# Performance work log

Hardware: AMD Instinct MI355X
Metric: run time of the kernel (lower is better)

Reference implementation:

```python
import jax, jax.numpy as jnp
import numpy as np

B, N, D = 8, 1024, 1024

def setup_inputs() -> dict:
    key = jax.random.key(0)
    k1, k2, k3, k4, k5 = jax.random.split(key, 5)
    x = jax.random.normal(k1, (B, N, D), dtype=jnp.float32)
    y = jax.random.normal(k2, (B, N, D), dtype=jnp.float32)
    adj = jax.random.uniform(k3, (B, N, N), dtype=jnp.float32)
    adj_sumrow = jnp.sum(adj, axis=-1, keepdims=True)  # [B, N, 1], row-sum normalizer
    W = jax.random.normal(k4, (D, D), dtype=jnp.float32) * (1.0 / np.sqrt(D))
    b = jax.random.normal(k5, (D,), dtype=jnp.float32) * 0.02
    return {"x": x, "y": y, "adj": adj, "adj_sumrow": adj_sumrow, "W": W, "b": b}

def reference(x, y, adj, adj_sumrow, W, b):
    # GraphConvolutionCustom: project neighbor features, aggregate via dense adj,
    # normalize by row-sum, add bias and residual input x; then ReLU.
    # Dropout is identity in eval mode (training=False).
    support = jnp.einsum('bnd,de->bne', y, W)          # [B, N, D]
    agg = jnp.matmul(adj, support) / adj_sumrow        # [B, N, D]
    out = jax.nn.relu(agg + b + x)
    return out
```

## Files before the change

### kernel.cpp

```cpp
#include <hip/hip_runtime.h>
#include <hip/hip_bf16.h>
#include <stdint.h>


typedef float  f32x4  __attribute__((ext_vector_type(4)));
typedef __bf16 bf16x8 __attribute__((ext_vector_type(8)));

__device__ __forceinline__ unsigned short f2bf(float f) {
  union { float f; unsigned int u; } c; c.f = f;
  unsigned int u = c.u;
  u += 0x7FFFu + ((u >> 16) & 1u);
  return (unsigned short)(u >> 16);
}

__device__ __forceinline__ void async_cp16(const void* g, void* l) {
  __builtin_amdgcn_global_load_lds(
      (const __attribute__((address_space(1))) unsigned int*)g,
      (__attribute__((address_space(3))) unsigned int*)l, 16, 0, 0);
}

__device__ __forceinline__ void bar() { asm volatile("s_barrier" ::: "memory"); }
#define VMCNT(n) asm volatile("s_waitcnt vmcnt(" #n ")" ::: "memory")


__global__ __launch_bounds__(256) void k_prep(
    const float4* __restrict__ y4, const float4* __restrict__ a4,
    ushort4* __restrict__ yb, ushort4* __restrict__ ab,
    const float* __restrict__ W, unsigned short* __restrict__ Wt)
{
  __shared__ float t[64][65];
  const int bid = blockIdx.x;
  if (bid < 16384) {
    const int i = bid * 256 + threadIdx.x;
    const bool isY = i < 2097152;
    const float4 v = isY ? y4[i] : a4[i - 2097152];
    ushort4 p;
    p.x = f2bf(v.x); p.y = f2bf(v.y); p.z = f2bf(v.z); p.w = f2bf(v.w);
    if (isY) yb[i] = p; else ab[i - 2097152] = p;
  } else {
    const int id = bid - 16384;
    const int n0 = (id & 15) * 64, k0 = (id >> 4) * 64;
    const int tx = threadIdx.x & 63, ty = threadIdx.x >> 6;
#pragma unroll
    for (int r = ty; r < 64; r += 4)
      t[r][tx] = W[(size_t)(k0 + r) * 1024 + n0 + tx];
    __syncthreads();
#pragma unroll
    for (int r = ty; r < 64; r += 4)
      Wt[(size_t)(n0 + r) * 1024 + k0 + tx] = f2bf(t[tx][r]);
  }
}


__device__ __forceinline__ void stageA(
    const unsigned short* __restrict__ A, int sA, int m0, int k0, int c,
    unsigned short* la, int wave, int rg, int colo)
{
#pragma unroll
  for (int s = 0; s < 2; ++s) {
    const int t = wave * 2 + s;
    const int row0 = (t >> 3) * 128 + c * 64 + (t & 7) * 8;
    async_cp16(A + (size_t)(m0 + row0 + rg) * sA + k0 + colo, la + row0 * 64);
  }
}

__device__ __forceinline__ void stageB(
    const unsigned short* __restrict__ Bt, int sB, int n0, int k0, int c,
    unsigned short* lb, int wave, int rg, int colo)
{
#pragma unroll
  for (int s = 0; s < 2; ++s) {
    const int t = wave * 2 + s;
    const int row0 = (t >> 2) * 64 + c * 32 + (t & 3) * 8;
    async_cp16(Bt + (size_t)(n0 + row0 + rg) * sB + k0 + colo, lb + row0 * 64);
  }
}

__device__ __forceinline__ void readA(
    const unsigned short* la, bf16x8 af[2][4], int wm, int mh, int quad, int l16)
{
#pragma unroll
  for (int h = 0; h < 2; ++h)
#pragma unroll
    for (int i = 0; i < 4; ++i) {
      const int r = wm + mh * 64 + i * 16 + l16;
      af[h][i] = *(const bf16x8*)(la + r * 64 + ((h * 4 + quad + r) & 7) * 8);
    }
}

__device__ __forceinline__ void readB(
    const unsigned short* lb, bf16x8 bfr[2][2], int wn, int nh, int quad, int l16)
{
#pragma unroll
  for (int h = 0; h < 2; ++h)
#pragma unroll
    for (int j = 0; j < 2; ++j) {
      const int r = wn + nh * 32 + j * 16 + l16;
      bfr[h][j] = *(const bf16x8*)(lb + r * 64 + ((h * 4 + quad + r) & 7) * 8);
    }
}

__device__ __forceinline__ void quad16(
    bf16x8 af[2][4], bf16x8 bfr[2][2], f32x4 acc[8][4], int mh, int nh)
{
  __builtin_amdgcn_s_setprio(1);
#pragma unroll
  for (int h = 0; h < 2; ++h)
#pragma unroll
    for (int i = 0; i < 4; ++i)
#pragma unroll
      for (int j = 0; j < 2; ++j)
        acc[mh * 4 + i][nh * 2 + j] = __builtin_amdgcn_mfma_f32_16x16x32_bf16(
            af[h][i], bfr[h][j], acc[mh * 4 + i][nh * 2 + j], 0, 0, 0);
  __builtin_amdgcn_s_setprio(0);
}

__device__ __forceinline__ void gemm256(
    const unsigned short* __restrict__ A,  int sA,
    const unsigned short* __restrict__ Bt, int sB,
    int m0, int n0, f32x4 acc[8][4], unsigned short* lsm, int tid)
{
  const int lane = tid & 63, wave = tid >> 6;
  const int wm = (wave >> 2) * 128, wn = (wave & 3) * 64;
  const int quad = lane >> 4, l16 = lane & 15;
  const int rg = lane >> 3;
  const int colo = (((lane & 7) - rg) & 7) * 8;

  bf16x8 af[2][4], bfr[2][2];

  stageA(A, sA, m0, 0, 0, lsm,        wave, rg, colo);
  stageB(Bt, sB, n0, 0, 0, lsm + 16384, wave, rg, colo);
  stageB(Bt, sB, n0, 0, 1, lsm + 16384, wave, rg, colo);
  stageA(A, sA, m0, 0, 1, lsm,        wave, rg, colo);

#pragma unroll 1
  for (int T = 0; T < 15; ++T) {
    const unsigned short* la = lsm + (T & 1) * 32768;
    const unsigned short* lb = la + 16384;
    unsigned short* na = lsm + ((T + 1) & 1) * 32768;
    unsigned short* nb = na + 16384;
    const int nk = (T + 1) * 64;

    VMCNT(4); bar();
    stageA(A, sA, m0, nk, 0, na, wave, rg, colo);
    readA(la, af, wm, 0, quad, l16);
    readB(lb, bfr, wn, 0, quad, l16);
    quad16(af, bfr, acc, 0, 0);

    VMCNT(4); bar();
    stageB(Bt, sB, n0, nk, 0, nb, wave, rg, colo);
    readB(lb, bfr, wn, 1, quad, l16);
    quad16(af, bfr, acc, 0, 1);

    VMCNT(4); bar();
    stageB(Bt, sB, n0, nk, 1, nb, wave, rg, colo);
    readA(la, af, wm, 1, quad, l16);
    quad16(af, bfr, acc, 1, 1);

    stageA(A, sA, m0, nk, 1, na, wave, rg, colo);
    readB(lb, bfr, wn, 0, quad, l16);
    quad16(af, bfr, acc, 1, 0);
  }

  {
    const unsigned short* la = lsm + 32768;
    const unsigned short* lb = la + 16384;
    VMCNT(4); bar();
    readA(la, af, wm, 0, quad, l16);
    readB(lb, bfr, wn, 0, quad, l16);
    quad16(af, bfr, acc, 0, 0);
    VMCNT(2); bar();
    readB(lb, bfr, wn, 1, quad, l16);
    quad16(af, bfr, acc, 0, 1);
    VMCNT(0); bar();
    readA(la, af, wm, 1, quad, l16);
    quad16(af, bfr, acc, 1, 1);
    readB(lb, bfr, wn, 0, quad, l16);
    quad16(af, bfr, acc, 1, 0);
  }
}

__device__ __forceinline__ void zero_acc(f32x4 acc[8][4]) {
#pragma unroll
  for (int i = 0; i < 8; ++i)
#pragma unroll
    for (int j = 0; j < 4; ++j)
#pragma unroll
      for (int r = 0; r < 4; ++r) acc[i][j][r] = 0.0f;
}


__global__ __launch_bounds__(512, 2) void k_gemm1(
    const unsigned short* __restrict__ Wt,
    const unsigned short* __restrict__ Ybf,
    unsigned short* __restrict__ Sup2)
{
  __shared__ __align__(16) unsigned short lsm[65536];
  const int tid = threadIdx.x;
  const int xcd = blockIdx.x & 7, slot = blockIdx.x >> 3;
  const int m0 = (slot >> 2) * 256;
  const int n0 = (xcd * 4 + (slot & 3)) * 256;

  f32x4 acc[8][4];
  zero_acc(acc);
  gemm256(Wt, 1024, Ybf, 1024, m0, n0, acc, lsm, tid);

  const int lane = tid & 63, wave = tid >> 6;
  const int wm = (wave >> 2) * 128, wn = (wave & 3) * 64;
  const int quad = lane >> 4, l16 = lane & 15;
#pragma unroll
  for (int mi = 0; mi < 8; ++mi) {
    const int mb = m0 + wm + mi * 16 + quad * 4;
#pragma unroll
    for (int r = 0; r < 4; ++r) {
      unsigned short* row = Sup2 + ((size_t)(mb + r) << 13);
#pragma unroll
      for (int nj = 0; nj < 4; ++nj)
        row[n0 + wn + nj * 16 + l16] = f2bf(acc[mi][nj][r]);
    }
  }
}


__global__ __launch_bounds__(512, 2) void k_gemm2(
    const unsigned short* __restrict__ AdjBf,
    const unsigned short* __restrict__ Sup2,
    const float* __restrict__ x,
    const float* __restrict__ sumrow,
    const float* __restrict__ bias,
    float* __restrict__ out)
{
  __shared__ __align__(16) unsigned short lsm[65536];
  const int tid = threadIdx.x;
  const int b = blockIdx.x & 7, slot = blockIdx.x >> 3;
  const int m0 = (slot >> 2) * 256, n0 = (slot & 3) * 256;

  f32x4 acc[8][4];
  zero_acc(acc);
  gemm256(AdjBf + ((size_t)b << 20), 1024,
          Sup2 + ((size_t)b << 10), 8192,
          m0, n0, acc, lsm, tid);

  const float* xb = x   + ((size_t)b << 20);
  float*       ob = out + ((size_t)b << 20);
  const float* sr = sumrow + ((size_t)b << 10);
  const int lane = tid & 63, wave = tid >> 6;
  const int wm = (wave >> 2) * 128, wn = (wave & 3) * 64;
  const int quad = lane >> 4, l16 = lane & 15;

  float bv[4];
#pragma unroll
  for (int nj = 0; nj < 4; ++nj) bv[nj] = bias[n0 + wn + nj * 16 + l16];

#pragma unroll
  for (int mi = 0; mi < 8; ++mi) {
    const int mb = m0 + wm + mi * 16 + quad * 4;
#pragma unroll
    for (int r = 0; r < 4; ++r) {
      const int m = mb + r;
      const float inv = 1.0f / sr[m];
#pragma unroll
      for (int nj = 0; nj < 4; ++nj) {
        const int n = n0 + wn + nj * 16 + l16;
        const size_t idx = (((size_t)m) << 10) + n;
        float v = acc[mi][nj][r] * inv + bv[nj] + xb[idx];
        ob[idx] = fmaxf(v, 0.0f);
      }
    }
  }
}


extern "C" void kernel_launch(void* const* d_in, const int* in_sizes, int n_in,
                              void* d_out, int out_size, void* d_ws, size_t ws_size,
                              hipStream_t stream) {
  const float* x      = (const float*)d_in[0];
  const float* y      = (const float*)d_in[1];
  const float* adj    = (const float*)d_in[2];
  const float* sumrow = (const float*)d_in[3];
  const float* W      = (const float*)d_in[4];
  const float* bias   = (const float*)d_in[5];
  float* out = (float*)d_out;

  char* ws = (char*)d_ws;
  unsigned short* ybf   = (unsigned short*)(ws);
  unsigned short* adjbf = (unsigned short*)(ws + ((size_t)16 << 20));
  unsigned short* wt    = (unsigned short*)(ws + ((size_t)32 << 20));
  unsigned short* sup2  = (unsigned short*)(ws + ((size_t)34 << 20));

  k_prep<<<dim3(16640), dim3(256), 0, stream>>>(
      (const float4*)y, (const float4*)adj, (ushort4*)ybf, (ushort4*)adjbf, W, wt);
  k_gemm1<<<dim3(128), dim3(512), 0, stream>>>(wt, ybf, sup2);
  k_gemm2<<<dim3(128), dim3(512), 0, stream>>>(adjbf, sup2, x, sumrow, bias, out);
}
```

Before: 223.8 us.

## Shrink GEMM tiles to 256x128 to launch 256 workgroups

Both GEMM kernels switch from 256x256 to 256x128 output tiles, doubling the grid from 128 to 256 workgroups so every CU on the device gets work. Each wave now owns a 64x64 sub-tile, the B staging loads a single 128-row chunk, and the LDS double buffer shrinks accordingly. The prefetch/barrier schedule is reworked to two waits per K step. This trades lower per-tile data reuse (more redundant loads of the A/B panels) for better occupancy and fewer accumulator registers.

```diff
diff --git a/kernel.cpp b/kernel.cpp
--- a/kernel.cpp
+++ b/kernel.cpp
@@ -59,31 +59,31 @@
 #pragma unroll
   for (int s = 0; s < 2; ++s) {
     const int t = wave * 2 + s;
-    const int row0 = (t >> 3) * 128 + c * 64 + (t & 7) * 8;
+    const int row0 = (t >> 2) * 64 + c * 32 + (t & 3) * 8;
     async_cp16(A + (size_t)(m0 + row0 + rg) * sA + k0 + colo, la + row0 * 64);
   }
 }
 
 __device__ __forceinline__ void stageB(
-    const unsigned short* __restrict__ Bt, int sB, int n0, int k0, int c,
+    const unsigned short* __restrict__ Bt, int sB, int n0, int k0,
     unsigned short* lb, int wave, int rg, int colo)
 {
 #pragma unroll
   for (int s = 0; s < 2; ++s) {
     const int t = wave * 2 + s;
-    const int row0 = (t >> 2) * 64 + c * 32 + (t & 3) * 8;
+    const int row0 = t * 8;
     async_cp16(Bt + (size_t)(n0 + row0 + rg) * sB + k0 + colo, lb + row0 * 64);
   }
 }
 
 __device__ __forceinline__ void readA(
-    const unsigned short* la, bf16x8 af[2][4], int wm, int mh, int quad, int l16)
+    const unsigned short* la, bf16x8 af[2][2], int wm, int mh, int quad, int l16)
 {
 #pragma unroll
   for (int h = 0; h < 2; ++h)
 #pragma unroll
-    for (int i = 0; i < 4; ++i) {
-      const int r = wm + mh * 64 + i * 16 + l16;
+    for (int i = 0; i < 2; ++i) {
+      const int r = wm + mh * 32 + i * 16 + l16;
       af[h][i] = *(const bf16x8*)(la + r * 64 + ((h * 4 + quad + r) & 7) * 8);
     }
 }
@@ -100,89 +100,85 @@
     }
 }
 
-__device__ __forceinline__ void quad16(
-    bf16x8 af[2][4], bf16x8 bfr[2][2], f32x4 acc[8][4], int mh, int nh)
+__device__ __forceinline__ void quad8(
+    bf16x8 af[2][2], bf16x8 bfr[2][2], f32x4 acc[4][4], int mh, int nh)
 {
   __builtin_amdgcn_s_setprio(1);
 #pragma unroll
   for (int h = 0; h < 2; ++h)
 #pragma unroll
-    for (int i = 0; i < 4; ++i)
+    for (int i = 0; i < 2; ++i)
 #pragma unroll
       for (int j = 0; j < 2; ++j)
-        acc[mh * 4 + i][nh * 2 + j] = __builtin_amdgcn_mfma_f32_16x16x32_bf16(
-            af[h][i], bfr[h][j], acc[mh * 4 + i][nh * 2 + j], 0, 0, 0);
+        acc[mh * 2 + i][nh * 2 + j] = __builtin_amdgcn_mfma_f32_16x16x32_bf16(
+            af[h][i], bfr[h][j], acc[mh * 2 + i][nh * 2 + j], 0, 0, 0);
   __builtin_amdgcn_s_setprio(0);
 }
 
-__device__ __forceinline__ void gemm256(
+__device__ __forceinline__ void gemm256x128(
     const unsigned short* __restrict__ A,  int sA,
     const unsigned short* __restrict__ Bt, int sB,
-    int m0, int n0, f32x4 acc[8][4], unsigned short* lsm, int tid)
+    int m0, int n0, f32x4 acc[4][4], unsigned short* lsm, int tid)
 {
   const int lane = tid & 63, wave = tid >> 6;
-  const int wm = (wave >> 2) * 128, wn = (wave & 3) * 64;
+  const int wm = (wave >> 1) * 64, wn = (wave & 1) * 64;
   const int quad = lane >> 4, l16 = lane & 15;
   const int rg = lane >> 3;
   const int colo = (((lane & 7) - rg) & 7) * 8;
 
-  bf16x8 af[2][4], bfr[2][2];
-
-  stageA(A, sA, m0, 0, 0, lsm,        wave, rg, colo);
-  stageB(Bt, sB, n0, 0, 0, lsm + 16384, wave, rg, colo);
-  stageB(Bt, sB, n0, 0, 1, lsm + 16384, wave, rg, colo);
-  stageA(A, sA, m0, 0, 1, lsm,        wave, rg, colo);
+  bf16x8 af[2][2], bfr[2][2];
+
+  stageA(A, sA, m0, 0, 0, lsm, wave, rg, colo);
+  stageB(Bt, sB, n0, 0, lsm + 16384, wave, rg, colo);
+  stageA(A, sA, m0, 0, 1, lsm, wave, rg, colo);
 
 #pragma unroll 1
   for (int T = 0; T < 15; ++T) {
-    const unsigned short* la = lsm + (T & 1) * 32768;
+    const unsigned short* la = lsm + (T & 1) * 24576;
     const unsigned short* lb = la + 16384;
-    unsigned short* na = lsm + ((T + 1) & 1) * 32768;
+    unsigned short* na = lsm + ((T + 1) & 1) * 24576;
     unsigned short* nb = na + 16384;
     const int nk = (T + 1) * 64;
 
-    VMCNT(4); bar();
     stageA(A, sA, m0, nk, 0, na, wave, rg, colo);
-    readA(la, af, wm, 0, quad, l16);
-    readB(lb, bfr, wn, 0, quad, l16);
-    quad16(af, bfr, acc, 0, 0);
-
-    VMCNT(4); bar();
-    stageB(Bt, sB, n0, nk, 0, nb, wave, rg, colo);
-    readB(lb, bfr, wn, 1, quad, l16);
-    quad16(af, bfr, acc, 0, 1);
-
-    VMCNT(4); bar();
-    stageB(Bt, sB, n0, nk, 1, nb, wave, rg, colo);
-    readA(la, af, wm, 1, quad, l16);
-    quad16(af, bfr, acc, 1, 1);
-
-    stageA(A, sA, m0, nk, 1, na, wave, rg, colo);
-    readB(lb, bfr, wn, 0, quad, l16);
-    quad16(af, bfr, acc, 1, 0);
-  }
-
-  {
-    const unsigned short* la = lsm + 32768;
-    const unsigned short* lb = la + 16384;
     VMCNT(4); bar();
     readA(la, af, wm, 0, quad, l16);
     readB(lb, bfr, wn, 0, quad, l16);
-    quad16(af, bfr, acc, 0, 0);
+    quad8(af, bfr, acc, 0, 0);
+
+    stageB(Bt, sB, n0, nk, nb, wave, rg, colo);
+    readB(lb, bfr, wn, 1, quad, l16);
+    quad8(af, bfr, acc, 0, 1);
+
+    stageA(A, sA, m0, nk, 1, na, wave, rg, colo);
+    VMCNT(6); bar();
+    readA(la, af, wm, 1, quad, l16);
+    quad8(af, bfr, acc, 1, 1);
+
+    readB(lb, bfr, wn, 0, quad, l16);
+    quad8(af, bfr, acc, 1, 0);
+  }
+
+  {
+    const unsigned short* la = lsm + 24576;
+    const unsigned short* lb = la + 16384;
     VMCNT(2); bar();
+    readA(la, af, wm, 0, quad, l16);
+    readB(lb, bfr, wn, 0, quad, l16);
+    quad8(af, bfr, acc, 0, 0);
     readB(lb, bfr, wn, 1, quad, l16);
-    quad16(af, bfr, acc, 0, 1);
+    quad8(af, bfr, acc, 0, 1);
     VMCNT(0); bar();
     readA(la, af, wm, 1, quad, l16);
-    quad16(af, bfr, acc, 1, 1);
-    readB(lb, bfr, wn, 0, quad, l16);
-    quad16(af, bfr, acc, 1, 0);
-  }
-}
-
-__device__ __forceinline__ void zero_acc(f32x4 acc[8][4]) {
-#pragma unroll
-  for (int i = 0; i < 8; ++i)
+    quad8(af, bfr, acc, 1, 1);
+    readB(lb, bfr, wn, 0, quad, l16);
+    quad8(af, bfr, acc, 1, 0);
+  }
+}
+
+__device__ __forceinline__ void zero_acc(f32x4 acc[4][4]) {
+#pragma unroll
+  for (int i = 0; i < 4; ++i)
 #pragma unroll
     for (int j = 0; j < 4; ++j)
 #pragma unroll
@@ -195,21 +191,21 @@
     const unsigned short* __restrict__ Ybf,
     unsigned short* __restrict__ Sup2)
 {
-  __shared__ __align__(16) unsigned short lsm[65536];
+  __shared__ __align__(16) unsigned short lsm[49152];
   const int tid = threadIdx.x;
   const int xcd = blockIdx.x & 7, slot = blockIdx.x >> 3;
-  const int m0 = (slot >> 2) * 256;
-  const int n0 = (xcd * 4 + (slot & 3)) * 256;
-
-  f32x4 acc[8][4];
+  const int m0 = (slot >> 3) * 256;
+  const int n0 = (xcd * 8 + (slot & 7)) * 128;
+
+  f32x4 acc[4][4];
   zero_acc(acc);
-  gemm256(Wt, 1024, Ybf, 1024, m0, n0, acc, lsm, tid);
+  gemm256x128(Wt, 1024, Ybf, 1024, m0, n0, acc, lsm, tid);
 
   const int lane = tid & 63, wave = tid >> 6;
-  const int wm = (wave >> 2) * 128, wn = (wave & 3) * 64;
+  const int wm = (wave >> 1) * 64, wn = (wave & 1) * 64;
   const int quad = lane >> 4, l16 = lane & 15;
 #pragma unroll
-  for (int mi = 0; mi < 8; ++mi) {
+  for (int mi = 0; mi < 4; ++mi) {
     const int mb = m0 + wm + mi * 16 + quad * 4;
 #pragma unroll
     for (int r = 0; r < 4; ++r) {
@@ -230,22 +226,22 @@
     const float* __restrict__ bias,
     float* __restrict__ out)
 {
-  __shared__ __align__(16) unsigned short lsm[65536];
+  __shared__ __align__(16) unsigned short lsm[49152];
   const int tid = threadIdx.x;
   const int b = blockIdx.x & 7, slot = blockIdx.x >> 3;
-  const int m0 = (slot >> 2) * 256, n0 = (slot & 3) * 256;
-
-  f32x4 acc[8][4];
+  const int m0 = (slot >> 3) * 256, n0 = (slot & 7) * 128;
+
+  f32x4 acc[4][4];
   zero_acc(acc);
-  gemm256(AdjBf + ((size_t)b << 20), 1024,
-          Sup2 + ((size_t)b << 10), 8192,
-          m0, n0, acc, lsm, tid);
+  gemm256x128(AdjBf + ((size_t)b << 20), 1024,
+              Sup2 + ((size_t)b << 10), 8192,
+              m0, n0, acc, lsm, tid);
 
   const float* xb = x   + ((size_t)b << 20);
   float*       ob = out + ((size_t)b << 20);
   const float* sr = sumrow + ((size_t)b << 10);
   const int lane = tid & 63, wave = tid >> 6;
-  const int wm = (wave >> 2) * 128, wn = (wave & 3) * 64;
+  const int wm = (wave >> 1) * 64, wn = (wave & 1) * 64;
   const int quad = lane >> 4, l16 = lane & 15;
 
   float bv[4];
@@ -253,7 +249,7 @@
   for (int nj = 0; nj < 4; ++nj) bv[nj] = bias[n0 + wn + nj * 16 + l16];
 
 #pragma unroll
-  for (int mi = 0; mi < 8; ++mi) {
+  for (int mi = 0; mi < 4; ++mi) {
     const int mb = m0 + wm + mi * 16 + quad * 4;
 #pragma unroll
     for (int r = 0; r < 4; ++r) {
@@ -290,6 +286,6 @@
 
   k_prep<<<dim3(16640), dim3(256), 0, stream>>>(
       (const float4*)y, (const float4*)adj, (ushort4*)ybf, (ushort4*)adjbf, W, wt);
-  k_gemm1<<<dim3(128), dim3(512), 0, stream>>>(wt, ybf, sup2);
-  k_gemm2<<<dim3(128), dim3(512), 0, stream>>>(adjbf, sup2, x, sumrow, bias, out);
-}
+  k_gemm1<<<dim3(256), dim3(512), 0, stream>>>(wt, ybf, sup2);
+  k_gemm2<<<dim3(256), dim3(512), 0, stream>>>(adjbf, sup2, x, sumrow, bias, out);
+}
```

Result: faster. 195.7 us (-12.6%).
